# Kernel optimization log

Measured on AMD Instinct MI355X. Metric: run time of the kernel, lower is better.

Reference implementation:

```python
import jax, jax.numpy as jnp
import numpy as np

B_, L_ = 32, 4096
D_MODEL, D_STATE, D_CONV, EXPAND, N_LAYERS, HORIZON = 128, 16, 4, 2, 4, 1
D_INNER = EXPAND * D_MODEL
DT_RANK = (D_MODEL + 15) // 16  # ceil(d_model/16) = 8
EPS = 1e-6


def setup_inputs() -> dict:
    key = jax.random.key(0)
    ks = jax.random.split(key, 10)
    s = lambda k, sh, sc: jax.random.normal(k, sh, jnp.float32) * sc
    inp = {}
    inp["x"] = s(ks[0], (B_, L_, 1), 1.0)
    inp["input_proj_w"] = s(ks[1], (D_MODEL, 1), 0.5)
    inp["input_proj_b"] = jnp.zeros((D_MODEL,), jnp.float32)
    inp["in_proj_w"] = s(ks[2], (N_LAYERS, 2 * D_INNER, D_MODEL), D_MODEL ** -0.5)
    inp["conv_w"] = s(ks[3], (N_LAYERS, D_INNER, 1, D_CONV), D_CONV ** -0.5)
    inp["conv_b"] = jnp.zeros((N_LAYERS, D_INNER), jnp.float32)
    inp["x_proj_w"] = s(ks[4], (N_LAYERS, DT_RANK + 2 * D_STATE, D_INNER), D_INNER ** -0.5)
    inp["dt_proj_w"] = s(ks[5], (N_LAYERS, D_INNER, DT_RANK), DT_RANK ** -0.5)
    inp["dt_proj_b"] = jnp.full((N_LAYERS, D_INNER), -4.0, jnp.float32)
    inp["A_log"] = jnp.tile(jnp.log(jnp.arange(1, D_STATE + 1, dtype=jnp.float32))[None, None, :], (N_LAYERS, D_INNER, 1))
    inp["D"] = jnp.ones((N_LAYERS, D_INNER), jnp.float32)
    inp["out_proj_w"] = s(ks[6], (N_LAYERS, D_MODEL, D_INNER), D_INNER ** -0.5)
    inp["norm_w"] = jnp.ones((D_MODEL,), jnp.float32)
    inp["output_proj_w"] = s(ks[7], (HORIZON, D_MODEL), D_MODEL ** -0.5)
    inp["output_proj_b"] = jnp.zeros((HORIZON,), jnp.float32)
    return inp


def _mamba_block(h, in_w, cw, cb, xpw, dtw, dtb, alog, d_skip, ow):
    # h: [B, L, d_model] -> [B, L, d_model]
    xz = jnp.einsum('bld,ed->ble', h, in_w)            # [B, L, 2*d_inner]
    x, z = jnp.split(xz, 2, axis=-1)                   # each [B, L, d_inner]
    # depthwise causal conv over time
    xc = jax.lax.conv_general_dilated(
        x.transpose(0, 2, 1), cw, window_strides=(1,),
        padding=[(D_CONV - 1, 0)], feature_group_count=D_INNER,
        dimension_numbers=('NCH', 'OIH', 'NCH'))      # [B, d_inner, L]
    x = jax.nn.silu(xc.transpose(0, 2, 1) + cb)        # [B, L, d_inner]
    dbl = jnp.einsum('blc,ec->ble', x, xpw)            # [B, L, dt_rank+2*d_state]
    dt, Bm, Cm = jnp.split(dbl, [DT_RANK, DT_RANK + D_STATE], axis=-1)
    dt = jax.nn.softplus(jnp.einsum('blr,cr->blc', dt, dtw) + dtb)  # [B, L, d_inner]
    A = -jnp.exp(alog)                                  # [d_inner, d_state]

    def step(hst, inputs):
        dt_t, B_t, C_t, x_t = inputs                   # [B,c],[B,s],[B,s],[B,c]
        hst = jnp.exp(dt_t[..., None] * A) * hst + (dt_t * x_t)[..., None] * B_t[:, None, :]
        y = jnp.einsum('bcs,bs->bc', hst, C_t)
        return hst, y

    h0 = jnp.zeros((x.shape[0], D_INNER, D_STATE), x.dtype)
    xs = (dt.transpose(1, 0, 2), Bm.transpose(1, 0, 2), Cm.transpose(1, 0, 2), x.transpose(1, 0, 2))
    _, ys = jax.lax.scan(step, h0, xs)                 # [L, B, d_inner]
    y = ys.transpose(1, 0, 2) + d_skip * x             # skip: y += D * x
    y = y * jax.nn.silu(z)                             # gating
    return jnp.einsum('blc,dc->bld', y, ow)            # [B, L, d_model]


def reference(x, input_proj_w, input_proj_b, in_proj_w, conv_w, conv_b, x_proj_w,
              dt_proj_w, dt_proj_b, A_log, D, out_proj_w, norm_w,
              output_proj_w, output_proj_b):
    h = jnp.einsum('blo,do->bld', x, input_proj_w) + input_proj_b  # [B, L, d_model]
    for i in range(N_LAYERS):
        h = h + _mamba_block(h, in_proj_w[i], conv_w[i], conv_b[i], x_proj_w[i],
                             dt_proj_w[i], dt_proj_b[i], A_log[i], D[i], out_proj_w[i])
    rms = jnp.sqrt(jnp.mean(h * h, axis=-1, keepdims=True) + EPS)
    h = norm_w * h / rms
    return h[:, -1, :] @ output_proj_w.T + output_proj_b  # [B, horizon]
```

## Files before the change

### kernel.cpp

```cpp
#include <hip/hip_runtime.h>

#define B_    32
#define L_    4096
#define DM    128
#define DI    256
#define DS_   16
#define RANK  8
#define NL    4
#define M_    (B_*L_)
#define NC    64
#define CL    (L_/NC)

typedef __attribute__((ext_vector_type(8))) short short8;
typedef __attribute__((ext_vector_type(4))) float floatx4;
typedef __attribute__((ext_vector_type(2))) float float2v;

__device__ __forceinline__ float b2f(unsigned short u) {
    return __uint_as_float(((unsigned)u) << 16);
}
__device__ __forceinline__ unsigned short f2b(float f) {
    unsigned u = __float_as_uint(f);
    unsigned r = u + 0x7fffu + ((u >> 16) & 1u);
    return (unsigned short)(r >> 16);
}
__device__ __forceinline__ float fast_sig(float v) {
    return __builtin_amdgcn_rcpf(1.f + __expf(-v));
}

__global__ __launch_bounds__(256) void k_detect(const unsigned short* __restrict__ x,
                                                int* __restrict__ flag) {
    __shared__ int cnt;
    if (threadIdx.x == 0) cnt = 0;
    __syncthreads();
    int ok = 0;
    for (int i = 0; i < 4; ++i) {
        unsigned short u = x[threadIdx.x * 4 + i];
        int e = (u >> 7) & 0xFF;
        if ((u & 0x7FFF) == 0 || (e >= 100 && e <= 150)) ok++;
    }
    atomicAdd(&cnt, ok);
    __syncthreads();
    if (threadIdx.x == 0) *flag = (cnt >= 800) ? 1 : 0;
}

struct CvtSeg { const void* src; float* dst; int n; };
struct CvtPack { CvtSeg seg[11]; };
__global__ __launch_bounds__(256) void k_cvt_params(CvtPack p, const int* __restrict__ flag) {
    int s = blockIdx.y;
    int i = blockIdx.x * 256 + threadIdx.x;
    if (i >= p.seg[s].n) return;
    p.seg[s].dst[i] = (*flag) ? b2f(((const unsigned short*)p.seg[s].src)[i])
                              : ((const float*)p.seg[s].src)[i];
}
__global__ __launch_bounds__(256) void k_cvt16(const void* __restrict__ src,
                                               unsigned short* __restrict__ dst,
                                               int n, const int* __restrict__ flag) {
    int i = blockIdx.x * 256 + threadIdx.x;
    if (i >= n) return;
    if (*flag) dst[i] = ((const unsigned short*)src)[i];
    else       dst[i] = f2b(((const float*)src)[i]);
}
__global__ __launch_bounds__(256) void k_xpw48(const void* __restrict__ src,
                                               unsigned short* __restrict__ dst,
                                               const int* __restrict__ flag) {
    int i = blockIdx.x * 256 + threadIdx.x;
    int col = i & 255, rowl = (i >> 8) % 48, layer = i / (48*256);
    unsigned short v = 0;
    if (rowl < 40) {
        int si = (layer*40 + rowl)*256 + col;
        v = (*flag) ? ((const unsigned short*)src)[si] : f2b(((const float*)src)[si]);
    }
    dst[i] = v;
}

__global__ __launch_bounds__(256) void k_init(const void* __restrict__ xraw,
                                              const int* __restrict__ flag,
                                              const float* __restrict__ ipw,
                                              const float* __restrict__ ipb,
                                              float* __restrict__ h, int base) {
    int idx = blockIdx.x * 256 + threadIdx.x;
    int bl = idx >> 7, d = idx & 127;
    float x = (*flag) ? b2f(((const unsigned short*)xraw)[base + bl])
                      : ((const float*)xraw)[base + bl];
    h[idx] = x * ipw[d] + ipb[d];
}

__global__ __launch_bounds__(256) void k_gemm_in(const float* __restrict__ h,
                                                 const unsigned short* __restrict__ w,
                                                 unsigned short* __restrict__ xb,
                                                 unsigned short* __restrict__ zb) {
    __shared__ unsigned short lA[64][136];
    __shared__ unsigned short lW[256][40];
    int tid = threadIdx.x;
    int lane = tid & 63, wv = tid >> 6;
    int ln = lane & 15, qd = lane >> 4;
    int r0 = blockIdx.x * 64;
    int n0 = blockIdx.y * 256;

    {
        int r = tid >> 2;
        int c0 = (tid & 3) * 32;
        const float4* src = (const float4*)(h + (size_t)(r0 + r) * DM + c0);
        for (int j = 0; j < 8; ++j) {
            float4 v = src[j];
            lA[r][c0 + j*4 + 0] = f2b(v.x);
            lA[r][c0 + j*4 + 1] = f2b(v.y);
            lA[r][c0 + j*4 + 2] = f2b(v.z);
            lA[r][c0 + j*4 + 3] = f2b(v.w);
        }
    }

    floatx4 acc[16];
    for (int i = 0; i < 16; ++i) acc[i] = (floatx4)0.f;

    for (int kc = 0; kc < 4; ++kc) {
        __syncthreads();
        {
            int n = tid;
            const uint4* src = (const uint4*)(w + (size_t)(n0 + n) * DM + kc * 32);
            uint4 a = src[0], b = src[1], c = src[2], d = src[3];
            *(uint4*)&lW[n][0]  = a;
            *(uint4*)&lW[n][8]  = b;
            *(uint4*)&lW[n][16] = c;
            *(uint4*)&lW[n][24] = d;
        }
        __syncthreads();
        short8 af = *(const short8*)&lA[wv*16 + ln][kc*32 + qd*8];
        for (int nt = 0; nt < 16; ++nt) {
            short8 bf = *(const short8*)&lW[nt*16 + ln][qd*8];
            acc[nt] = __builtin_amdgcn_mfma_f32_16x16x32_bf16(af, bf, acc[nt], 0, 0, 0);
        }
    }

    for (int nt = 0; nt < 16; ++nt)
        for (int rg = 0; rg < 4; ++rg) {
            size_t gr = (size_t)(r0 + wv*16 + qd*4 + rg);
            int gc = nt*16 + ln;
            unsigned short v = f2b(acc[nt][rg]);
            if (blockIdx.y == 0) xb[gr*DI + gc] = v;
            else                 zb[gr*DI + gc] = v;
        }
}

__global__ __launch_bounds__(256) void k_xprojc(const unsigned short* __restrict__ xb,
                                                const float* __restrict__ cw,
                                                const float* __restrict__ cbp,
                                                const unsigned short* __restrict__ w48,
                                                const float* __restrict__ dtw,
                                                const float* __restrict__ dtb,
                                                unsigned short* __restrict__ xcg,
                                                unsigned short* __restrict__ dtg,
                                                unsigned short* __restrict__ Bg,
                                                unsigned short* __restrict__ Cg) {
    __shared__ unsigned short lA[64][264];
    __shared__ unsigned short lW[48][40];
    __shared__ float ldbl[64][8];
    int tid = threadIdx.x;
    int lane = tid & 63, wv = tid >> 6;
    int ln = lane & 15, qd = lane >> 4;
    int r0 = blockIdx.x * 64;
    int l0 = r0 & (L_ - 1);

    {
        int c = tid;
        float w0 = cw[c*4+0], w1 = cw[c*4+1], w2 = cw[c*4+2], w3 = cw[c*4+3];
        float bias = cbp[c];
        float x0 = (l0 >= 3) ? b2f(xb[(size_t)(r0-3)*DI + c]) : 0.f;
        float x1 = (l0 >= 2) ? b2f(xb[(size_t)(r0-2)*DI + c]) : 0.f;
        float x2 = (l0 >= 1) ? b2f(xb[(size_t)(r0-1)*DI + c]) : 0.f;
        for (int r = 0; r < 64; ++r) {
            float xcur = b2f(xb[(size_t)(r0+r)*DI + c]);
            float v = w0*x0 + w1*x1 + w2*x2 + w3*xcur + bias;
            float s = v * fast_sig(v);
            unsigned short sb = f2b(s);
            lA[r][c] = sb;
            xcg[(size_t)(r0+r)*DI + c] = sb;
            x0 = x1; x1 = x2; x2 = xcur;
        }
    }

    floatx4 acc[3];
    for (int i = 0; i < 3; ++i) acc[i] = (floatx4)0.f;

    for (int kc = 0; kc < 8; ++kc) {
        __syncthreads();
        if (tid < 192) {
            int n = tid >> 2, q = tid & 3;
            *(uint4*)&lW[n][q*8] = *(const uint4*)(w48 + (size_t)n*DI + kc*32 + q*8);
        }
        __syncthreads();
        short8 af = *(const short8*)&lA[wv*16 + ln][kc*32 + qd*8];
        for (int nt = 0; nt < 3; ++nt) {
            short8 bf = *(const short8*)&lW[nt*16 + ln][qd*8];
            acc[nt] = __builtin_amdgcn_mfma_f32_16x16x32_bf16(af, bf, acc[nt], 0, 0, 0);
        }
    }

    for (int nt = 0; nt < 3; ++nt)
        for (int rg = 0; rg < 4; ++rg) {
            int rloc = wv*16 + qd*4 + rg;
            size_t row = (size_t)(r0 + rloc);
            int n = nt*16 + ln;
            float v = acc[nt][rg];
            if (n < 8)       ldbl[rloc][n] = v;
            else if (n < 24) Bg[row*DS_ + (n-8)]  = f2b(v);
            else if (n < 40) Cg[row*DS_ + (n-24)] = f2b(v);
        }
    __syncthreads();

    {
        int c = tid;
        float w8[8];
        #pragma unroll
        for (int j = 0; j < 8; ++j) w8[j] = dtw[c*8 + j];
        float bias = dtb[c];
        for (int r = 0; r < 64; ++r) {
            float a = bias;
            #pragma unroll
            for (int j = 0; j < 8; ++j) a += ldbl[r][j] * w8[j];
            float sp = (a > 20.f) ? a : __logf(1.f + __expf(a));
            dtg[(size_t)(r0+r)*DI + c] = f2b(sp);
        }
    }
}

__device__ __forceinline__ bool a_is_integer_ladder(const float* A) {
    bool f = true;
    #pragma unroll
    for (int s = 0; s < DS_; ++s)
        f = f && (fabsf(A[s] + (float)(s+1)) < 0.01f * (float)(s+1));
    return f;
}

__device__ __forceinline__ void unpack8(uint4 p, float* f) {
    f[0] = b2f((unsigned short)(p.x & 0xffff)); f[1] = b2f((unsigned short)(p.x >> 16));
    f[2] = b2f((unsigned short)(p.y & 0xffff)); f[3] = b2f((unsigned short)(p.y >> 16));
    f[4] = b2f((unsigned short)(p.z & 0xffff)); f[5] = b2f((unsigned short)(p.z >> 16));
    f[6] = b2f((unsigned short)(p.w & 0xffff)); f[7] = b2f((unsigned short)(p.w >> 16));
}

__global__ __launch_bounds__(256) void k_scan1(const unsigned short* __restrict__ dtg,
                                               const unsigned short* __restrict__ xcg,
                                               const unsigned short* __restrict__ Bg,
                                               const float* __restrict__ alog,
                                               float* __restrict__ Pbuf,
                                               float* __restrict__ Hbuf) {
    __shared__ float lB[CL*DS_];
    int c = threadIdx.x;
    int k = blockIdx.x, b = blockIdx.y;
    size_t row0 = (size_t)b * L_ + (size_t)k * CL;
    if (c < 128) {
        uint4 p = ((const uint4*)(Bg + row0*DS_))[c];
        float f[8]; unpack8(p, f);
        *(float4*)&lB[c*8]     = make_float4(f[0], f[1], f[2], f[3]);
        *(float4*)&lB[c*8 + 4] = make_float4(f[4], f[5], f[6], f[7]);
    }
    float A[DS_];
    #pragma unroll
    for (int j = 0; j < 4; ++j) {
        float4 a4 = *(const float4*)(alog + c*DS_ + j*4);
        A[j*4+0] = -__expf(a4.x); A[j*4+1] = -__expf(a4.y);
        A[j*4+2] = -__expf(a4.z); A[j*4+3] = -__expf(a4.w);
    }
    __syncthreads();
    const unsigned short* pdt = dtg + row0*DI + c;
    const unsigned short* pxc = xcg + row0*DI + c;
    float dtc = b2f(*pdt), xcc = b2f(*pxc);
    float P[DS_];

    if (a_is_integer_ladder(A)) {
        float2v h2[8];
        #pragma unroll
        for (int j = 0; j < 8; ++j) h2[j] = (float2v)0.f;
        float S = 0.f;
        for (int l = 0; l < CL; ++l) {
            float dtn = b2f(pdt[DI]); float xcn = b2f(pxc[DI]);
            float du = dtc * xcc;
            float Bl[DS_];
            *(float4*)&Bl[0]  = *(const float4*)&lB[l*DS_ + 0];
            *(float4*)&Bl[4]  = *(const float4*)&lB[l*DS_ + 4];
            *(float4*)&Bl[8]  = *(const float4*)&lB[l*DS_ + 8];
            *(float4*)&Bl[12] = *(const float4*)&lB[l*DS_ + 12];
            float E = __expf(-dtc);
            float E2 = E * E;
            float2v ep[8];
            ep[0].x = E; ep[0].y = E2;
            float2v E22; E22.x = E2; E22.y = E2;
            #pragma unroll
            for (int j = 1; j < 8; ++j) ep[j] = ep[j-1] * E22;
            float2v du2; du2.x = du; du2.y = du;
            #pragma unroll
            for (int j = 0; j < 8; ++j) {
                float2v bj; bj.x = Bl[2*j]; bj.y = Bl[2*j+1];
                h2[j] = ep[j]*h2[j] + du2*bj;
            }
            S += dtc;
            dtc = dtn; xcc = xcn; pdt += DI; pxc += DI;
        }
        #pragma unroll
        for (int s = 0; s < DS_; ++s) P[s] = __expf(-(float)(s+1) * S);
        float4* pp = (float4*)(Pbuf + (((size_t)b*NC + k)*DI + c)*DS_);
        float4* ph = (float4*)(Hbuf + (((size_t)b*NC + k)*DI + c)*DS_);
        #pragma unroll
        for (int j = 0; j < 4; ++j) {
            pp[j] = make_float4(P[j*4+0], P[j*4+1], P[j*4+2], P[j*4+3]);
            ph[j] = make_float4(h2[j*2].x, h2[j*2].y, h2[j*2+1].x, h2[j*2+1].y);
        }
    } else {
        float h[DS_];
        #pragma unroll
        for (int s = 0; s < DS_; ++s) { h[s] = 0.f; P[s] = 1.f; }
        for (int l = 0; l < CL; ++l) {
            float dtn = b2f(pdt[DI]); float xcn = b2f(pxc[DI]);
            float du = dtc * xcc;
            float Bl[DS_];
            *(float4*)&Bl[0]  = *(const float4*)&lB[l*DS_ + 0];
            *(float4*)&Bl[4]  = *(const float4*)&lB[l*DS_ + 4];
            *(float4*)&Bl[8]  = *(const float4*)&lB[l*DS_ + 8];
            *(float4*)&Bl[12] = *(const float4*)&lB[l*DS_ + 12];
            #pragma unroll
            for (int s = 0; s < DS_; ++s) {
                float e = __expf(dtc * A[s]);
                h[s] = e*h[s] + du*Bl[s];
                P[s] *= e;
            }
            dtc = dtn; xcc = xcn; pdt += DI; pxc += DI;
        }
        float4* pp = (float4*)(Pbuf + (((size_t)b*NC + k)*DI + c)*DS_);
        float4* ph = (float4*)(Hbuf + (((size_t)b*NC + k)*DI + c)*DS_);
        #pragma unroll
        for (int j = 0; j < 4; ++j) {
            pp[j] = make_float4(P[j*4+0], P[j*4+1], P[j*4+2], P[j*4+3]);
            ph[j] = make_float4(h[j*4+0], h[j*4+1], h[j*4+2], h[j*4+3]);
        }
    }
}

__global__ __launch_bounds__(256) void k_scan2(const float* __restrict__ Pbuf,
                                               float* __restrict__ Hbuf,
                                               int cb) {
    int t = blockIdx.x * 256 + threadIdx.x;
    if (t >= cb * DI * DS_) return;
    int b  = t / (DI * DS_);
    int cs = t % (DI * DS_);
    float H = 0.f;
    for (int k = 0; k < NC; ++k) {
        size_t idx = ((size_t)b * NC + k) * (DI * DS_) + cs;
        float P  = Pbuf[idx];
        float he = Hbuf[idx];
        Hbuf[idx] = H;
        H = P * H + he;
    }
}

__global__ __launch_bounds__(256) void k_scan3g(const unsigned short* __restrict__ dtg,
                                                const unsigned short* __restrict__ xcg,
                                                const unsigned short* __restrict__ Bg,
                                                const unsigned short* __restrict__ Cg,
                                                const float* __restrict__ alog,
                                                const float* __restrict__ Hbuf,
                                                const unsigned short* __restrict__ zb,
                                                const float* __restrict__ Dp,
                                                unsigned short* __restrict__ yg) {
    __shared__ float lB[CL*DS_];
    __shared__ float lC[CL*DS_];
    int c = threadIdx.x;
    int k = blockIdx.x, b = blockIdx.y;
    size_t row0 = (size_t)b * L_ + (size_t)k * CL;
    {
        int t = c & 127;
        const unsigned short* src = (c < 128) ? (Bg + row0*DS_) : (Cg + row0*DS_);
        float* dst = (c < 128) ? lB : lC;
        uint4 p = ((const uint4*)src)[t];
        float f[8]; unpack8(p, f);
        *(float4*)&dst[t*8]     = make_float4(f[0], f[1], f[2], f[3]);
        *(float4*)&dst[t*8 + 4] = make_float4(f[4], f[5], f[6], f[7]);
    }
    float A[DS_];
    #pragma unroll
    for (int j = 0; j < 4; ++j) {
        float4 a4 = *(const float4*)(alog + c*DS_ + j*4);
        A[j*4+0] = -__expf(a4.x); A[j*4+1] = -__expf(a4.y);
        A[j*4+2] = -__expf(a4.z); A[j*4+3] = -__expf(a4.w);
    }
    float Dc = Dp[c];
    __syncthreads();
    const unsigned short* pdt = dtg + row0*DI + c;
    const unsigned short* pxc = xcg + row0*DI + c;
    const unsigned short* pz  = zb  + row0*DI + c;
    unsigned short* py        = yg  + row0*DI + c;
    float dtc = b2f(*pdt), xcc = b2f(*pxc), zc = b2f(*pz);

    if (a_is_integer_ladder(A)) {
        float2v h2[8];
        {
            const float4* ph = (const float4*)(Hbuf + (((size_t)b*NC + k)*DI + c)*DS_);
            #pragma unroll
            for (int j = 0; j < 4; ++j) {
                float4 v = ph[j];
                h2[j*2].x = v.x; h2[j*2].y = v.y;
                h2[j*2+1].x = v.z; h2[j*2+1].y = v.w;
            }
        }
        for (int l = 0; l < CL; ++l) {
            float dtn = b2f(pdt[DI]); float xcn = b2f(pxc[DI]); float zn = b2f(pz[DI]);
            float du = dtc * xcc;
            float Bl[DS_], Cl[DS_];
            *(float4*)&Bl[0]  = *(const float4*)&lB[l*DS_ + 0];
            *(float4*)&Bl[4]  = *(const float4*)&lB[l*DS_ + 4];
            *(float4*)&Bl[8]  = *(const float4*)&lB[l*DS_ + 8];
            *(float4*)&Bl[12] = *(const float4*)&lB[l*DS_ + 12];
            *(float4*)&Cl[0]  = *(const float4*)&lC[l*DS_ + 0];
            *(float4*)&Cl[4]  = *(const float4*)&lC[l*DS_ + 4];
            *(float4*)&Cl[8]  = *(const float4*)&lC[l*DS_ + 8];
            *(float4*)&Cl[12] = *(const float4*)&lC[l*DS_ + 12];
            float E = __expf(-dtc);
            float E2 = E * E;
            float2v ep[8];
            ep[0].x = E; ep[0].y = E2;
            float2v E22; E22.x = E2; E22.y = E2;
            #pragma unroll
            for (int j = 1; j < 8; ++j) ep[j] = ep[j-1] * E22;
            float2v du2; du2.x = du; du2.y = du;
            float2v y2 = (float2v)0.f;
            #pragma unroll
            for (int j = 0; j < 8; ++j) {
                float2v bj; bj.x = Bl[2*j]; bj.y = Bl[2*j+1];
                float2v cj; cj.x = Cl[2*j]; cj.y = Cl[2*j+1];
                h2[j] = ep[j]*h2[j] + du2*bj;
                y2 = y2 + h2[j]*cj;
            }
            float y = y2.x + y2.y;
            *py = f2b((y + Dc*xcc) * (zc * fast_sig(zc)));
            dtc = dtn; xcc = xcn; zc = zn;
            pdt += DI; pxc += DI; pz += DI; py += DI;
        }
    } else {
        float h[DS_];
        {
            const float4* ph = (const float4*)(Hbuf + (((size_t)b*NC + k)*DI + c)*DS_);
            #pragma unroll
            for (int j = 0; j < 4; ++j) {
                float4 v = ph[j];
                h[j*4+0] = v.x; h[j*4+1] = v.y; h[j*4+2] = v.z; h[j*4+3] = v.w;
            }
        }
        for (int l = 0; l < CL; ++l) {
            float dtn = b2f(pdt[DI]); float xcn = b2f(pxc[DI]); float zn = b2f(pz[DI]);
            float du = dtc * xcc;
            float Bl[DS_], Cl[DS_];
            *(float4*)&Bl[0]  = *(const float4*)&lB[l*DS_ + 0];
            *(float4*)&Bl[4]  = *(const float4*)&lB[l*DS_ + 4];
            *(float4*)&Bl[8]  = *(const float4*)&lB[l*DS_ + 8];
            *(float4*)&Bl[12] = *(const float4*)&lB[l*DS_ + 12];
            *(float4*)&Cl[0]  = *(const float4*)&lC[l*DS_ + 0];
            *(float4*)&Cl[4]  = *(const float4*)&lC[l*DS_ + 4];
            *(float4*)&Cl[8]  = *(const float4*)&lC[l*DS_ + 8];
            *(float4*)&Cl[12] = *(const float4*)&lC[l*DS_ + 12];
            float y = 0.f;
            #pragma unroll
            for (int s = 0; s < DS_; ++s) {
                float e = __expf(dtc * A[s]);
                h[s] = e*h[s] + du*Bl[s];
                y += h[s]*Cl[s];
            }
            *py = f2b((y + Dc*xcc) * (zc * fast_sig(zc)));
            dtc = dtn; xcc = xcn; zc = zn;
            pdt += DI; pxc += DI; pz += DI; py += DI;
        }
    }
}

__global__ __launch_bounds__(256) void k_gemm_out(const unsigned short* __restrict__ yg,
                                                  const unsigned short* __restrict__ w,
                                                  float* __restrict__ h) {
    __shared__ unsigned short lA[64][264];
    __shared__ unsigned short lW[128][40];
    int tid = threadIdx.x;
    int lane = tid & 63, wv = tid >> 6;
    int ln = lane & 15, qd = lane >> 4;
    int r0 = blockIdx.x * 64;

    for (int j = 0; j < 8; ++j) {
        int idx = tid + j*256;
        int r = idx >> 5, q = idx & 31;
        *(uint4*)&lA[r][q*8] = *(const uint4*)(yg + (size_t)(r0 + r)*DI + q*8);
    }

    floatx4 acc[8];
    for (int i = 0; i < 8; ++i) acc[i] = (floatx4)0.f;

    for (int kc = 0; kc < 8; ++kc) {
        __syncthreads();
        {
            int n = tid >> 1, half = tid & 1;
            const uint4* src = (const uint4*)(w + (size_t)n*DI + kc*32 + half*16);
            uint4 a = src[0], b4 = src[1];
            *(uint4*)&lW[n][half*16]     = a;
            *(uint4*)&lW[n][half*16 + 8] = b4;
        }
        __syncthreads();
        short8 af = *(const short8*)&lA[wv*16 + ln][kc*32 + qd*8];
        for (int nt = 0; nt < 8; ++nt) {
            short8 bf = *(const short8*)&lW[nt*16 + ln][qd*8];
            acc[nt] = __builtin_amdgcn_mfma_f32_16x16x32_bf16(af, bf, acc[nt], 0, 0, 0);
        }
    }

    for (int nt = 0; nt < 8; ++nt)
        for (int rg = 0; rg < 4; ++rg) {
            size_t gr = (size_t)(r0 + wv*16 + qd*4 + rg);
            int gc = nt*16 + ln;
            h[gr*DM + gc] += acc[nt][rg];
        }
}

__global__ __launch_bounds__(128) void k_head(const float* __restrict__ h,
                                              const float* __restrict__ nw,
                                              const float* __restrict__ opw,
                                              const float* __restrict__ opb,
                                              float* __restrict__ out) {
    __shared__ float red[4];
    int b = blockIdx.x, d = threadIdx.x;
    float hv = h[((size_t)b*L_ + (L_-1))*DM + d];
    float v = hv * hv;
    for (int off = 1; off < 64; off <<= 1) v += __shfl_xor(v, off);
    if ((d & 63) == 0) red[d >> 6] = v;
    __syncthreads();
    float ss = red[0] + red[1];
    float rms = sqrtf(ss * (1.f/DM) + 1e-6f);
    float hn = nw[d] * hv / rms;
    float pv = hn * opw[d];
    for (int off = 1; off < 64; off <<= 1) pv += __shfl_xor(pv, off);
    if ((d & 63) == 0) red[2 + (d >> 6)] = pv;
    __syncthreads();
    if (d == 0) out[b] = red[2] + red[3] + opb[0];
}

extern "C" void kernel_launch(void* const* d_in, const int* in_sizes, int n_in,
                              void* d_out, int out_size, void* d_ws, size_t ws_size,
                              hipStream_t stream) {
    (void)in_sizes; (void)n_in; (void)out_size;
    float* out = (float*)d_out;

    char* wp = (char*)d_ws;
    int* flag = (int*)wp; wp += 16;
    auto allocf = [&](size_t elems) {
        float* p = (float*)wp;
        wp += (elems * 4 + 15) & ~(size_t)15;
        return p;
    };
    auto alloch = [&](size_t elems) {
        unsigned short* p = (unsigned short*)wp;
        wp += (elems * 2 + 15) & ~(size_t)15;
        return p;
    };
    float* c_ipw  = allocf(DM);
    float* c_ipb  = allocf(DM);
    float* c_cw   = allocf((size_t)NL*DI*4);
    float* c_cb   = allocf((size_t)NL*DI);
    float* c_dtw  = allocf((size_t)NL*DI*RANK);
    float* c_dtb  = allocf((size_t)NL*DI);
    float* c_alog = allocf((size_t)NL*DI*DS_);
    float* c_D    = allocf((size_t)NL*DI);
    float* c_nw   = allocf(DM);
    float* c_opw  = allocf(DM);
    float* c_opb  = allocf(1);
    unsigned short* c_inw16 = alloch((size_t)NL*2*DI*DM);
    unsigned short* c_ow16  = alloch((size_t)NL*DM*DI);
    unsigned short* c_xpw48 = alloch((size_t)NL*48*DI);
    wp = (char*)(((size_t)wp + 255) & ~(size_t)255);

    k_detect<<<1, 256, 0, stream>>>((const unsigned short*)d_in[0], flag);

    CvtPack pk;
    pk.seg[0]  = { d_in[1],  c_ipw,  DM };
    pk.seg[1]  = { d_in[2],  c_ipb,  DM };
    pk.seg[2]  = { d_in[4],  c_cw,   NL*DI*4 };
    pk.seg[3]  = { d_in[5],  c_cb,   NL*DI };
    pk.seg[4]  = { d_in[7],  c_dtw,  NL*DI*RANK };
    pk.seg[5]  = { d_in[8],  c_dtb,  NL*DI };
    pk.seg[6]  = { d_in[9],  c_alog, NL*DI*DS_ };
    pk.seg[7]  = { d_in[10], c_D,    NL*DI };
    pk.seg[8]  = { d_in[12], c_nw,   DM };
    pk.seg[9]  = { d_in[13], c_opw,  DM };
    pk.seg[10] = { d_in[14], c_opb,  1 };
    k_cvt_params<<<dim3(64, 11), 256, 0, stream>>>(pk, flag);
    k_cvt16<<<(int)((NL*2*DI*DM + 255)/256), 256, 0, stream>>>(d_in[3],  c_inw16, NL*2*DI*DM, flag);
    k_cvt16<<<(int)((NL*DM*DI   + 255)/256), 256, 0, stream>>>(d_in[11], c_ow16,  NL*DM*DI,   flag);
    k_xpw48<<<NL*48*DI/256, 256, 0, stream>>>(d_in[6], c_xpw48, flag);

    size_t used  = (size_t)(wp - (char*)d_ws);
    size_t avail = (ws_size > used) ? ws_size - used : 0;
    const size_t perB = (size_t)L_ * 2624 + (size_t)2 * NC * DI * DS_ * 4;
    int cb = B_;
    while (cb > 1 && (size_t)cb * perB > avail) cb >>= 1;
    const int Mc = cb * L_;

    float* h            = (float*)wp;          wp += (size_t)Mc*DM*4;
    unsigned short* xb  = (unsigned short*)wp; wp += (size_t)Mc*DI*2;
    unsigned short* zb  = (unsigned short*)wp; wp += (size_t)Mc*DI*2;
    unsigned short* xcg = (unsigned short*)wp; wp += (size_t)Mc*DI*2;
    unsigned short* dty = (unsigned short*)wp; wp += (size_t)Mc*DI*2;
    unsigned short* Bg  = (unsigned short*)wp; wp += (size_t)Mc*DS_*2;
    unsigned short* Cg  = (unsigned short*)wp; wp += (size_t)Mc*DS_*2;
    float* Pbuf         = (float*)wp;          wp += (size_t)cb*NC*DI*DS_*4;
    float* Hbuf         = (float*)wp;          wp += (size_t)cb*NC*DI*DS_*4;

    const int scan2_blocks = (cb * DI * DS_ + 255) / 256;

    for (int b0 = 0; b0 < B_; b0 += cb) {
        k_init<<<Mc*DM/256, 256, 0, stream>>>(d_in[0], flag, c_ipw, c_ipb, h, b0*L_);
        for (int i = 0; i < NL; ++i) {
            k_gemm_in<<<dim3(Mc/64, 2), 256, 0, stream>>>(h, c_inw16 + (size_t)i*2*DI*DM, xb, zb);
            k_xprojc<<<Mc/64, 256, 0, stream>>>(xb, c_cw + i*DI*4, c_cb + i*DI,
                                                c_xpw48 + (size_t)i*48*DI,
                                                c_dtw + i*DI*RANK, c_dtb + i*DI,
                                                xcg, dty, Bg, Cg);
            k_scan1<<<dim3(NC, cb), 256, 0, stream>>>(dty, xcg, Bg, c_alog + i*DI*DS_, Pbuf, Hbuf);
            k_scan2<<<scan2_blocks, 256, 0, stream>>>(Pbuf, Hbuf, cb);
            k_scan3g<<<dim3(NC, cb), 256, 0, stream>>>(dty, xcg, Bg, Cg, c_alog + i*DI*DS_,
                                                       Hbuf, zb, c_D + i*DI, xb);
            k_gemm_out<<<Mc/64, 256, 0, stream>>>(xb, c_ow16 + (size_t)i*DM*DI, h);
        }
        k_head<<<cb, 128, 0, stream>>>(h, c_nw, c_opw, c_opb, out + b0);
    }
}
```

Before: 1.530 ms.

## Fuse chunk-local scan pass into x-projection/conv kernel

Removes the separate k_scan1 launch and computes each 64-row chunk's local state and decay product inside k_xprojc. It reuses the conv output, B and dt values already held in shared memory and registers instead of re-reading them from global memory. This relies on the block tile (64 rows) matching the chunk length CL, and it lengthens the per-thread serial work in the projection kernel, which may raise register pressure.

```diff
diff --git a/kernel.cpp b/kernel.cpp
--- a/kernel.cpp
+++ b/kernel.cpp
@@ -142,24 +142,45 @@
         }
 }
 
+__device__ __forceinline__ bool a_is_integer_ladder(const float* A) {
+    bool f = true;
+    #pragma unroll
+    for (int s = 0; s < DS_; ++s)
+        f = f && (fabsf(A[s] + (float)(s+1)) < 0.01f * (float)(s+1));
+    return f;
+}
+
+__device__ __forceinline__ void unpack8(uint4 p, float* f) {
+    f[0] = b2f((unsigned short)(p.x & 0xffff)); f[1] = b2f((unsigned short)(p.x >> 16));
+    f[2] = b2f((unsigned short)(p.y & 0xffff)); f[3] = b2f((unsigned short)(p.y >> 16));
+    f[4] = b2f((unsigned short)(p.z & 0xffff)); f[5] = b2f((unsigned short)(p.z >> 16));
+    f[6] = b2f((unsigned short)(p.w & 0xffff)); f[7] = b2f((unsigned short)(p.w >> 16));
+}
+
 __global__ __launch_bounds__(256) void k_xprojc(const unsigned short* __restrict__ xb,
                                                 const float* __restrict__ cw,
                                                 const float* __restrict__ cbp,
                                                 const unsigned short* __restrict__ w48,
                                                 const float* __restrict__ dtw,
                                                 const float* __restrict__ dtb,
+                                                const float* __restrict__ alog,
                                                 unsigned short* __restrict__ xcg,
                                                 unsigned short* __restrict__ dtg,
                                                 unsigned short* __restrict__ Bg,
-                                                unsigned short* __restrict__ Cg) {
+                                                unsigned short* __restrict__ Cg,
+                                                float* __restrict__ Pbuf,
+                                                float* __restrict__ Hbuf) {
     __shared__ unsigned short lA[64][264];
     __shared__ unsigned short lW[48][40];
     __shared__ float ldbl[64][8];
+    __shared__ float lBs[64][DS_];
     int tid = threadIdx.x;
     int lane = tid & 63, wv = tid >> 6;
     int ln = lane & 15, qd = lane >> 4;
     int r0 = blockIdx.x * 64;
     int l0 = r0 & (L_ - 1);
+    int bidx = r0 >> 12;
+    int kidx = l0 >> 6;
 
     {
         int c = tid;
@@ -203,7 +224,11 @@
             int n = nt*16 + ln;
             float v = acc[nt][rg];
             if (n < 8)       ldbl[rloc][n] = v;
-            else if (n < 24) Bg[row*DS_ + (n-8)]  = f2b(v);
+            else if (n < 24) {
+                unsigned short bv = f2b(v);
+                Bg[row*DS_ + (n-8)] = bv;
+                lBs[rloc][n-8] = b2f(bv);
+            }
             else if (n < 40) Cg[row*DS_ + (n-24)] = f2b(v);
         }
     __syncthreads();
@@ -214,124 +239,89 @@
         #pragma unroll
         for (int j = 0; j < 8; ++j) w8[j] = dtw[c*8 + j];
         float bias = dtb[c];
-        for (int r = 0; r < 64; ++r) {
-            float a = bias;
-            #pragma unroll
-            for (int j = 0; j < 8; ++j) a += ldbl[r][j] * w8[j];
-            float sp = (a > 20.f) ? a : __logf(1.f + __expf(a));
-            dtg[(size_t)(r0+r)*DI + c] = f2b(sp);
-        }
-    }
-}
-
-__device__ __forceinline__ bool a_is_integer_ladder(const float* A) {
-    bool f = true;
-    #pragma unroll
-    for (int s = 0; s < DS_; ++s)
-        f = f && (fabsf(A[s] + (float)(s+1)) < 0.01f * (float)(s+1));
-    return f;
-}
-
-__device__ __forceinline__ void unpack8(uint4 p, float* f) {
-    f[0] = b2f((unsigned short)(p.x & 0xffff)); f[1] = b2f((unsigned short)(p.x >> 16));
-    f[2] = b2f((unsigned short)(p.y & 0xffff)); f[3] = b2f((unsigned short)(p.y >> 16));
-    f[4] = b2f((unsigned short)(p.z & 0xffff)); f[5] = b2f((unsigned short)(p.z >> 16));
-    f[6] = b2f((unsigned short)(p.w & 0xffff)); f[7] = b2f((unsigned short)(p.w >> 16));
-}
-
-__global__ __launch_bounds__(256) void k_scan1(const unsigned short* __restrict__ dtg,
-                                               const unsigned short* __restrict__ xcg,
-                                               const unsigned short* __restrict__ Bg,
-                                               const float* __restrict__ alog,
-                                               float* __restrict__ Pbuf,
-                                               float* __restrict__ Hbuf) {
-    __shared__ float lB[CL*DS_];
-    int c = threadIdx.x;
-    int k = blockIdx.x, b = blockIdx.y;
-    size_t row0 = (size_t)b * L_ + (size_t)k * CL;
-    if (c < 128) {
-        uint4 p = ((const uint4*)(Bg + row0*DS_))[c];
-        float f[8]; unpack8(p, f);
-        *(float4*)&lB[c*8]     = make_float4(f[0], f[1], f[2], f[3]);
-        *(float4*)&lB[c*8 + 4] = make_float4(f[4], f[5], f[6], f[7]);
-    }
-    float A[DS_];
-    #pragma unroll
-    for (int j = 0; j < 4; ++j) {
-        float4 a4 = *(const float4*)(alog + c*DS_ + j*4);
-        A[j*4+0] = -__expf(a4.x); A[j*4+1] = -__expf(a4.y);
-        A[j*4+2] = -__expf(a4.z); A[j*4+3] = -__expf(a4.w);
-    }
-    __syncthreads();
-    const unsigned short* pdt = dtg + row0*DI + c;
-    const unsigned short* pxc = xcg + row0*DI + c;
-    float dtc = b2f(*pdt), xcc = b2f(*pxc);
-    float P[DS_];
-
-    if (a_is_integer_ladder(A)) {
-        float2v h2[8];
-        #pragma unroll
-        for (int j = 0; j < 8; ++j) h2[j] = (float2v)0.f;
-        float S = 0.f;
-        for (int l = 0; l < CL; ++l) {
-            float dtn = b2f(pdt[DI]); float xcn = b2f(pxc[DI]);
-            float du = dtc * xcc;
-            float Bl[DS_];
-            *(float4*)&Bl[0]  = *(const float4*)&lB[l*DS_ + 0];
-            *(float4*)&Bl[4]  = *(const float4*)&lB[l*DS_ + 4];
-            *(float4*)&Bl[8]  = *(const float4*)&lB[l*DS_ + 8];
-            *(float4*)&Bl[12] = *(const float4*)&lB[l*DS_ + 12];
-            float E = __expf(-dtc);
-            float E2 = E * E;
-            float2v ep[8];
-            ep[0].x = E; ep[0].y = E2;
-            float2v E22; E22.x = E2; E22.y = E2;
-            #pragma unroll
-            for (int j = 1; j < 8; ++j) ep[j] = ep[j-1] * E22;
-            float2v du2; du2.x = du; du2.y = du;
-            #pragma unroll
-            for (int j = 0; j < 8; ++j) {
-                float2v bj; bj.x = Bl[2*j]; bj.y = Bl[2*j+1];
-                h2[j] = ep[j]*h2[j] + du2*bj;
-            }
-            S += dtc;
-            dtc = dtn; xcc = xcn; pdt += DI; pxc += DI;
-        }
-        #pragma unroll
-        for (int s = 0; s < DS_; ++s) P[s] = __expf(-(float)(s+1) * S);
-        float4* pp = (float4*)(Pbuf + (((size_t)b*NC + k)*DI + c)*DS_);
-        float4* ph = (float4*)(Hbuf + (((size_t)b*NC + k)*DI + c)*DS_);
+        float A[DS_];
         #pragma unroll
         for (int j = 0; j < 4; ++j) {
-            pp[j] = make_float4(P[j*4+0], P[j*4+1], P[j*4+2], P[j*4+3]);
-            ph[j] = make_float4(h2[j*2].x, h2[j*2].y, h2[j*2+1].x, h2[j*2+1].y);
-        }
-    } else {
-        float h[DS_];
-        #pragma unroll
-        for (int s = 0; s < DS_; ++s) { h[s] = 0.f; P[s] = 1.f; }
-        for (int l = 0; l < CL; ++l) {
-            float dtn = b2f(pdt[DI]); float xcn = b2f(pxc[DI]);
-            float du = dtc * xcc;
-            float Bl[DS_];
-            *(float4*)&Bl[0]  = *(const float4*)&lB[l*DS_ + 0];
-            *(float4*)&Bl[4]  = *(const float4*)&lB[l*DS_ + 4];
-            *(float4*)&Bl[8]  = *(const float4*)&lB[l*DS_ + 8];
-            *(float4*)&Bl[12] = *(const float4*)&lB[l*DS_ + 12];
-            #pragma unroll
-            for (int s = 0; s < DS_; ++s) {
-                float e = __expf(dtc * A[s]);
-                h[s] = e*h[s] + du*Bl[s];
-                P[s] *= e;
-            }
-            dtc = dtn; xcc = xcn; pdt += DI; pxc += DI;
-        }
-        float4* pp = (float4*)(Pbuf + (((size_t)b*NC + k)*DI + c)*DS_);
-        float4* ph = (float4*)(Hbuf + (((size_t)b*NC + k)*DI + c)*DS_);
-        #pragma unroll
-        for (int j = 0; j < 4; ++j) {
-            pp[j] = make_float4(P[j*4+0], P[j*4+1], P[j*4+2], P[j*4+3]);
-            ph[j] = make_float4(h[j*4+0], h[j*4+1], h[j*4+2], h[j*4+3]);
+            float4 a4 = *(const float4*)(alog + c*DS_ + j*4);
+            A[j*4+0] = -__expf(a4.x); A[j*4+1] = -__expf(a4.y);
+            A[j*4+2] = -__expf(a4.z); A[j*4+3] = -__expf(a4.w);
+        }
+        float P[DS_];
+        if (a_is_integer_ladder(A)) {
+            float2v h2[8];
+            #pragma unroll
+            for (int j = 0; j < 8; ++j) h2[j] = (float2v)0.f;
+            float S = 0.f;
+            for (int r = 0; r < 64; ++r) {
+                float a = bias;
+                #pragma unroll
+                for (int j = 0; j < 8; ++j) a += ldbl[r][j] * w8[j];
+                float sp = (a > 20.f) ? a : __logf(1.f + __expf(a));
+                unsigned short spb = f2b(sp);
+                dtg[(size_t)(r0+r)*DI + c] = spb;
+                float dtv = b2f(spb);
+                float du = dtv * b2f(lA[r][c]);
+                float Bl[DS_];
+                *(float4*)&Bl[0]  = *(const float4*)&lBs[r][0];
+                *(float4*)&Bl[4]  = *(const float4*)&lBs[r][4];
+                *(float4*)&Bl[8]  = *(const float4*)&lBs[r][8];
+                *(float4*)&Bl[12] = *(const float4*)&lBs[r][12];
+                float E = __expf(-dtv);
+                float E2 = E * E;
+                float2v ep[8];
+                ep[0].x = E; ep[0].y = E2;
+                float2v E22; E22.x = E2; E22.y = E2;
+                #pragma unroll
+                for (int j = 1; j < 8; ++j) ep[j] = ep[j-1] * E22;
+                float2v du2; du2.x = du; du2.y = du;
+                #pragma unroll
+                for (int j = 0; j < 8; ++j) {
+                    float2v bj; bj.x = Bl[2*j]; bj.y = Bl[2*j+1];
+                    h2[j] = ep[j]*h2[j] + du2*bj;
+                }
+                S += dtv;
+            }
+            #pragma unroll
+            for (int s = 0; s < DS_; ++s) P[s] = __expf(-(float)(s+1) * S);
+            float4* pp = (float4*)(Pbuf + (((size_t)bidx*NC + kidx)*DI + c)*DS_);
+            float4* ph = (float4*)(Hbuf + (((size_t)bidx*NC + kidx)*DI + c)*DS_);
+            #pragma unroll
+            for (int j = 0; j < 4; ++j) {
+                pp[j] = make_float4(P[j*4+0], P[j*4+1], P[j*4+2], P[j*4+3]);
+                ph[j] = make_float4(h2[j*2].x, h2[j*2].y, h2[j*2+1].x, h2[j*2+1].y);
+            }
+        } else {
+            float h[DS_];
+            #pragma unroll
+            for (int s = 0; s < DS_; ++s) { h[s] = 0.f; P[s] = 1.f; }
+            for (int r = 0; r < 64; ++r) {
+                float a = bias;
+                #pragma unroll
+                for (int j = 0; j < 8; ++j) a += ldbl[r][j] * w8[j];
+                float sp = (a > 20.f) ? a : __logf(1.f + __expf(a));
+                unsigned short spb = f2b(sp);
+                dtg[(size_t)(r0+r)*DI + c] = spb;
+                float dtv = b2f(spb);
+                float du = dtv * b2f(lA[r][c]);
+                float Bl[DS_];
+                *(float4*)&Bl[0]  = *(const float4*)&lBs[r][0];
+                *(float4*)&Bl[4]  = *(const float4*)&lBs[r][4];
+                *(float4*)&Bl[8]  = *(const float4*)&lBs[r][8];
+                *(float4*)&Bl[12] = *(const float4*)&lBs[r][12];
+                #pragma unroll
+                for (int s = 0; s < DS_; ++s) {
+                    float e = __expf(dtv * A[s]);
+                    h[s] = e*h[s] + du*Bl[s];
+                    P[s] *= e;
+                }
+            }
+            float4* pp = (float4*)(Pbuf + (((size_t)bidx*NC + kidx)*DI + c)*DS_);
+            float4* ph = (float4*)(Hbuf + (((size_t)bidx*NC + kidx)*DI + c)*DS_);
+            #pragma unroll
+            for (int j = 0; j < 4; ++j) {
+                pp[j] = make_float4(P[j*4+0], P[j*4+1], P[j*4+2], P[j*4+3]);
+                ph[j] = make_float4(h[j*4+0], h[j*4+1], h[j*4+2], h[j*4+3]);
+            }
         }
     }
 }
@@ -616,8 +606,8 @@
             k_xprojc<<<Mc/64, 256, 0, stream>>>(xb, c_cw + i*DI*4, c_cb + i*DI,
                                                 c_xpw48 + (size_t)i*48*DI,
                                                 c_dtw + i*DI*RANK, c_dtb + i*DI,
-                                                xcg, dty, Bg, Cg);
-            k_scan1<<<dim3(NC, cb), 256, 0, stream>>>(dty, xcg, Bg, c_alog + i*DI*DS_, Pbuf, Hbuf);
+                                                c_alog + i*DI*DS_,
+                                                xcg, dty, Bg, Cg, Pbuf, Hbuf);
             k_scan2<<<scan2_blocks, 256, 0, stream>>>(Pbuf, Hbuf, cb);
             k_scan3g<<<dim3(NC, cb), 256, 0, stream>>>(dty, xcg, Bg, Cg, c_alog + i*DI*DS_,
                                                        Hbuf, zb, c_D + i*DI, xb);
```

New measurement: 1.496 ms. 1.02x faster.
